# Kernel optimization log

Hardware: AMD Instinct MI355X
Metric: run time of the kernel (lower is better)

The kernel has to match this reference:

```python
import jax, jax.numpy as jnp
import numpy as np

S_SCALE = 40.0  # ReuseThreshold default s
EPS = 0.0  # torch .norm division has no eps; keep faithful


def _monotonic_threshold(param):
    # get_monotonic_threshold with use_sigmoid=True: squash raw param into (0, 1)
    return jax.nn.sigmoid(param)


def setup_inputs() -> dict:
    key = jax.random.key(0)
    k1, k2, k3, k4, k5 = jax.random.split(key, 5)
    B, N, D = 16, 2048, 768
    return {
        "query_input": jax.random.normal(k1, (B, N, D), dtype=jnp.float32),
        "query_value": jax.random.normal(k2, (B, N, D), dtype=jnp.float32),
        "cached_input": jax.random.normal(k3, (B, N, D), dtype=jnp.float32),
        "cached_value": jax.random.normal(k4, (B, N, D), dtype=jnp.float32),
        "sim_threshold": jax.random.normal(k5, (N,), dtype=jnp.float32),
    }


def reference(query_input, query_value, cached_input, cached_value, sim_threshold):
    # L2-normalize along feature dim
    nq = query_input / jnp.linalg.norm(query_input, axis=-1, keepdims=True)
    nc = cached_input / jnp.linalg.norm(cached_input, axis=-1, keepdims=True)
    # full similarity matrix [B, N, N], top-1 retrieval
    sim = jnp.einsum("bnd,bmd->bnm", nq, nc)
    most_similar_score = jnp.max(sim, axis=-1)          # [B, N]
    most_similar_idx = jnp.argmax(sim, axis=-1)         # [B, N]
    idx = most_similar_idx[..., None]                   # [B, N, 1]
    similar_input = jnp.take_along_axis(cached_input, idx, axis=1)  # [B, N, D]
    similar_value = jnp.take_along_axis(cached_value, idx, axis=1)
    # learned sigmoid threshold blend
    threshold = _monotonic_threshold(sim_threshold)     # [N]
    reuse_map = jax.nn.sigmoid(S_SCALE * (most_similar_score - threshold))  # [B, N]
    rm = reuse_map[..., None]
    reuse_input = (1.0 - rm) * query_input + rm * similar_input
    reuse_value = (1.0 - rm) * query_value + rm * similar_value
    return (reuse_map, reuse_input, reuse_value)
```

## Files before the change

kernel.cpp:

```cpp
#include <hip/hip_runtime.h>
#include <stdint.h>

#define BB 16
#define NN 2048
#define DD 768
#define BN (BB*NN)
#define NCH (DD/32)


typedef __attribute__((ext_vector_type(8))) short bf16x8;
typedef __attribute__((ext_vector_type(4))) float f32x4;

__device__ __forceinline__ ushort f2bf_rne(float x) {
    uint32_t u = __float_as_uint(x);
    u += 0x7fffu + ((u >> 16) & 1u);
    return (ushort)(u >> 16);
}

__device__ __forceinline__ void gload16(const void* g, void* l) {
    __builtin_amdgcn_global_load_lds(
        (const __attribute__((address_space(1))) void*)g,
        (__attribute__((address_space(3))) void*)l,
        16, 0, 0);
}

__global__ __launch_bounds__(256) void normconv_kernel(
        const float* __restrict__ qi, const float* __restrict__ ci,
        ushort* __restrict__ qh, ushort* __restrict__ ql,
        ushort* __restrict__ ch, ushort* __restrict__ cl) {
    const int gw   = blockIdx.x * 4 + (threadIdx.x >> 6);
    const int lane = threadIdx.x & 63;
#pragma unroll
    for (int it = 0; it < 8; it++) {
        int row = gw + it * 8192;
        bool isq = row < BN;
        const float* src = isq ? qi : ci;
        int r = row & (BN - 1);
        const float4* p = (const float4*)(src + (size_t)r * DD);
        float4 v[3];
        float s = 0.0f;
#pragma unroll
        for (int k = 0; k < 3; k++) {
            v[k] = p[lane + 64 * k];
            s += v[k].x*v[k].x + v[k].y*v[k].y + v[k].z*v[k].z + v[k].w*v[k].w;
        }
#pragma unroll
        for (int off = 32; off; off >>= 1) s += __shfl_xor(s, off);
        float inv = 1.0f / sqrtf(s);
        ushort* dh = (isq ? qh : ch) + (size_t)r * DD;
        ushort* dl = (isq ? ql : cl) + (size_t)r * DD;
#pragma unroll
        for (int k = 0; k < 3; k++) {
            int f = lane + 64 * k;
            float n[4] = {v[k].x * inv, v[k].y * inv, v[k].z * inv, v[k].w * inv};
            ushort hs[4], ls[4];
#pragma unroll
            for (int e = 0; e < 4; e++) {
                hs[e] = f2bf_rne(n[e]);
                ls[e] = f2bf_rne(n[e] - __uint_as_float((uint32_t)hs[e] << 16));
            }
            uint2 hv, lv;
            hv.x = (uint32_t)hs[0] | ((uint32_t)hs[1] << 16);
            hv.y = (uint32_t)hs[2] | ((uint32_t)hs[3] << 16);
            lv.x = (uint32_t)ls[0] | ((uint32_t)ls[1] << 16);
            lv.y = (uint32_t)ls[2] | ((uint32_t)ls[3] << 16);
            *(uint2*)(dh + 4 * (size_t)f) = hv;
            *(uint2*)(dl + 4 * (size_t)f) = lv;
        }
    }
}

__global__ __launch_bounds__(256, 2) void simmax_kernel(
        const ushort* __restrict__ qh, const ushort* __restrict__ ql,
        const ushort* __restrict__ ch, const ushort* __restrict__ cl,
        float* __restrict__ pmax, int* __restrict__ pidx) {
    __shared__ ushort smem[2][4][128 * 32];
    __shared__ float  redm[2][128];
    __shared__ int    redi[2][128];

    const int t  = threadIdx.x;
    const int l  = t & 63, wid = t >> 6;
    const int wy = wid >> 1, wx = wid & 1;
    const int fr = l & 15,  fs = l >> 4;
    const int n0 = blockIdx.x * 128;
    const int ms = blockIdx.y;
    const int b  = blockIdx.z;
    const int n0g = b * NN + n0;

    const int rowl = l >> 2;
    const int gs   = (l & 3) ^ ((l >> 3) & 3);
    const int rb   = wid * 32;

    const int swz = (fs ^ ((fr >> 1) & 3)) * 8;
    const int ra0 = (wy * 64 + fr) * 32 + swz;
    const int rb0 = (wx * 64 + fr) * 32 + swz;

    const ushort* srcs[4] = {qh, ql, ch, cl};

    float rmax[16]; int ridx[16];
#pragma unroll
    for (int k = 0; k < 16; k++) { rmax[k] = -3.0e38f; ridx[k] = 0; }

    for (int mt = ms; mt < 16; mt += 4) {
        const int m0  = mt * 128;
        const int m0g = b * NN + m0;

        f32x4 acc[4][4];
#pragma unroll
        for (int i = 0; i < 4; i++)
#pragma unroll
            for (int j = 0; j < 4; j++)
#pragma unroll
                for (int r = 0; r < 4; r++) acc[i][j][r] = 0.0f;

#pragma unroll
        for (int a = 0; a < 4; a++) {
            const ushort* sp = srcs[a]
                + (size_t)((a < 2 ? n0g : m0g) + rb + rowl) * DD + gs * 8;
            ushort* lp = &smem[0][a][rb * 32];
            gload16(sp, lp);
            gload16(sp + 16 * DD, lp + 16 * 32);
        }
        __syncthreads();

        int cur = 0;
        for (int c = 0; c < NCH; c++) {
            if (c + 1 < NCH) {
                const int k1 = (c + 1) * 32;
#pragma unroll
                for (int a = 0; a < 4; a++) {
                    const ushort* sp = srcs[a]
                        + (size_t)((a < 2 ? n0g : m0g) + rb + rowl) * DD
                        + k1 + gs * 8;
                    ushort* lp = &smem[cur ^ 1][a][rb * 32];
                    gload16(sp, lp);
                    gload16(sp + 16 * DD, lp + 16 * 32);
                }
            }
            bf16x8 ah[4], al[4], bhf[4], blf[4];
#pragma unroll
            for (int i = 0; i < 4; i++) {
                ah[i]  = *(const bf16x8*)&smem[cur][0][ra0 + i * 512];
                al[i]  = *(const bf16x8*)&smem[cur][1][ra0 + i * 512];
                bhf[i] = *(const bf16x8*)&smem[cur][2][rb0 + i * 512];
                blf[i] = *(const bf16x8*)&smem[cur][3][rb0 + i * 512];
            }
#pragma unroll
            for (int i = 0; i < 4; i++)
#pragma unroll
                for (int j = 0; j < 4; j++) {
                    asm("v_mfma_f32_16x16x32_bf16 %0, %1, %2, %0"
                        : "+v"(acc[i][j]) : "v"(ah[i]), "v"(bhf[j]));
                    asm("v_mfma_f32_16x16x32_bf16 %0, %1, %2, %0"
                        : "+v"(acc[i][j]) : "v"(al[i]), "v"(bhf[j]));
                    asm("v_mfma_f32_16x16x32_bf16 %0, %1, %2, %0"
                        : "+v"(acc[i][j]) : "v"(ah[i]), "v"(blf[j]));
                }
            __syncthreads();
            cur ^= 1;
        }

#pragma unroll
        for (int j = 0; j < 4; j++) {
            const int col = m0 + wx * 64 + j * 16 + fr;
#pragma unroll
            for (int i = 0; i < 4; i++)
#pragma unroll
                for (int r = 0; r < 4; r++) {
                    float val = acc[i][j][r];
                    int k = i * 4 + r;
                    if (val > rmax[k]) { rmax[k] = val; ridx[k] = col; }
                }
        }
    }

#pragma unroll
    for (int k = 0; k < 16; k++) {
        float m = rmax[k]; int id2 = ridx[k];
#pragma unroll
        for (int off = 1; off < 16; off <<= 1) {
            float om = __shfl_xor(m, off);
            int   oi = __shfl_xor(id2, off);
            if (om > m || (om == m && oi < id2)) { m = om; id2 = oi; }
        }
        if (fr == 0) {
            int r_loc = wy * 64 + (k >> 2) * 16 + fs * 4 + (k & 3);
            redm[wx][r_loc] = m;
            redi[wx][r_loc] = id2;
        }
    }
    __syncthreads();
    if (t < 128) {
        float m0v = redm[0][t]; int i0 = redi[0][t];
        float m1v = redm[1][t]; int i1 = redi[1][t];
        if (m1v > m0v || (m1v == m0v && i1 < i0)) { m0v = m1v; i0 = i1; }
        pmax[(b * 4 + ms) * NN + n0 + t] = m0v;
        pidx[(b * 4 + ms) * NN + n0 + t] = i0;
    }
}

__global__ __launch_bounds__(256) void blend_kernel(
        const float* __restrict__ qi, const float* __restrict__ qv,
        const float* __restrict__ ci, const float* __restrict__ cv,
        const float* __restrict__ pmax, const int* __restrict__ pidx,
        const float* __restrict__ st,
        float* __restrict__ out_map,
        float* __restrict__ out_ri, float* __restrict__ out_rv) {
    const int gw   = blockIdx.x * 4 + (threadIdx.x >> 6);
    const int lane = threadIdx.x & 63;

    float pm[4]; int pi[4];
    {
        int b = gw >> 11, n = gw & 2047;
#pragma unroll
        for (int s = 0; s < 4; s++) {
            pm[s] = pmax[(b * 4 + s) * NN + n];
            pi[s] = pidx[(b * 4 + s) * NN + n];
        }
    }

#pragma unroll
    for (int i = 0; i < 4; i++) {
        const int row = gw + i * 8192;
        const int b = row >> 11, n = row & 2047;

        float best = pm[0]; int bi = pi[0];
#pragma unroll
        for (int s = 1; s < 4; s++)
            if (pm[s] > best || (pm[s] == best && pi[s] < bi)) {
                best = pm[s]; bi = pi[s];
            }
        float thr = 1.0f / (1.0f + expf(-st[n]));
        float rm  = 1.0f / (1.0f + expf(-40.0f * (best - thr)));

        if (i < 3) {
            int rown = gw + (i + 1) * 8192;
            int bn_ = rown >> 11, nn_ = rown & 2047;
#pragma unroll
            for (int s = 0; s < 4; s++) {
                pm[s] = pmax[(bn_ * 4 + s) * NN + nn_];
                pi[s] = pidx[(bn_ * 4 + s) * NN + nn_];
            }
        }

        if (lane == 0) out_map[row] = rm;
        const float om = 1.0f - rm;
        const float4* q4 = (const float4*)(qi + (size_t)row * DD);
        const float4* v4 = (const float4*)(qv + (size_t)row * DD);
        const float4* s4 = (const float4*)(ci + ((size_t)b * NN + bi) * DD);
        const float4* w4 = (const float4*)(cv + ((size_t)b * NN + bi) * DD);
        float4* ori = (float4*)(out_ri + (size_t)row * DD);
        float4* orv = (float4*)(out_rv + (size_t)row * DD);
#pragma unroll
        for (int k = 0; k < 3; k++) {
            int f = lane + 64 * k;
            float4 a = q4[f], si = s4[f];
            float4 o;
            o.x = om * a.x + rm * si.x;
            o.y = om * a.y + rm * si.y;
            o.z = om * a.z + rm * si.z;
            o.w = om * a.w + rm * si.w;
            ori[f] = o;
            float4 av = v4[f], sv = w4[f];
            float4 p;
            p.x = om * av.x + rm * sv.x;
            p.y = om * av.y + rm * sv.y;
            p.z = om * av.z + rm * sv.z;
            p.w = om * av.w + rm * sv.w;
            orv[f] = p;
        }
    }
}

extern "C" void kernel_launch(void* const* d_in, const int* in_sizes, int n_in,
                              void* d_out, int out_size, void* d_ws, size_t ws_size,
                              hipStream_t stream) {
    const float* qi = (const float*)d_in[0];
    const float* qv = (const float*)d_in[1];
    const float* ci = (const float*)d_in[2];
    const float* cv = (const float*)d_in[3];
    const float* st = (const float*)d_in[4];

    float* ws    = (float*)d_ws;
    float* pmax  = ws;
    int*   pidx  = (int*)(ws + 131072);

    float* out     = (float*)d_out;
    float* out_map = out;
    float* out_ri  = out + 32768;
    float* out_rv  = out + 32768 + (size_t)BN * DD;

    ushort* qh = (ushort*)out_ri;
    ushort* ql = qh + (size_t)BN * DD;
    ushort* ch = (ushort*)out_rv;
    ushort* cl = ch + (size_t)BN * DD;

    normconv_kernel<<<2048, 256, 0, stream>>>(qi, ci, qh, ql, ch, cl);
    dim3 g2(16, 4, BB);
    simmax_kernel<<<g2, 256, 0, stream>>>(qh, ql, ch, cl, pmax, pidx);
    blend_kernel<<<2048, 256, 0, stream>>>(qi, qv, ci, cv, pmax, pidx, st,
                                           out_map, out_ri, out_rv);
}
```

Before: 821.2 us.

## Enlarge similarity GEMM tile to 256x256 with 8 waves and quarter-phased pipelining

The sim-max GEMM moves from 128x128 tiles with 4 waves to 256x256 tiles with 8 waves. Each K step is split into four MFMA phases, with the next tile's global-to-LDS loads interleaved between them, and s_setprio raised around the MFMA work. The prefetch now runs across M-tile boundaries so the pipeline does not drain between tiles. The larger tile halves global reloads per output and halves the number of M partials the blend kernel has to merge. In exchange it needs more registers and LDS per block, and the grid shrinks to 256 blocks, which may underfill the CUs.

```diff
diff --git a/kernel.cpp b/kernel.cpp
--- a/kernel.cpp
+++ b/kernel.cpp
@@ -5,7 +5,6 @@
 #define NN 2048
 #define DD 768
 #define BN (BB*NN)
-#define NCH (DD/32)
 
 
 typedef __attribute__((ext_vector_type(8))) short bf16x8;
@@ -70,133 +69,216 @@
     }
 }
 
-__global__ __launch_bounds__(256, 2) void simmax_kernel(
+__global__ __launch_bounds__(512, 2) void simmax_kernel(
         const ushort* __restrict__ qh, const ushort* __restrict__ ql,
         const ushort* __restrict__ ch, const ushort* __restrict__ cl,
         float* __restrict__ pmax, int* __restrict__ pidx) {
-    __shared__ ushort smem[2][4][128 * 32];
-    __shared__ float  redm[2][128];
-    __shared__ int    redi[2][128];
-
-    const int t  = threadIdx.x;
-    const int l  = t & 63, wid = t >> 6;
-    const int wy = wid >> 1, wx = wid & 1;
-    const int fr = l & 15,  fs = l >> 4;
-    const int n0 = blockIdx.x * 128;
-    const int ms = blockIdx.y;
-    const int b  = blockIdx.z;
+    __shared__ ushort sA[2][2][256 * 32];
+    __shared__ ushort sB[2][2][256 * 32];
+    __shared__ float  redm[4][256];
+    __shared__ int    redi[4][256];
+
+    const int t   = threadIdx.x;
+    const int l   = t & 63, wid = t >> 6;
+    const int wy  = wid >> 2, wx = wid & 3;
+    const int fr  = l & 15,  fs = l >> 4;
+    const int n0  = blockIdx.x * 256;
+    const int ms  = blockIdx.y;
+    const int b   = blockIdx.z;
     const int n0g = b * NN + n0;
 
     const int rowl = l >> 2;
     const int gs   = (l & 3) ^ ((l >> 3) & 3);
-    const int rb   = wid * 32;
-
-    const int swz = (fs ^ ((fr >> 1) & 3)) * 8;
-    const int ra0 = (wy * 64 + fr) * 32 + swz;
-    const int rb0 = (wx * 64 + fr) * 32 + swz;
-
-    const ushort* srcs[4] = {qh, ql, ch, cl};
-
-    float rmax[16]; int ridx[16];
-#pragma unroll
-    for (int k = 0; k < 16; k++) { rmax[k] = -3.0e38f; ridx[k] = 0; }
-
-    for (int mt = ms; mt < 16; mt += 4) {
-        const int m0  = mt * 128;
+    const int wr16 = wid * 16;
+
+    const int psl = (fs ^ ((fr >> 1) & 3)) * 8;
+    const int rA  = (wy * 128 + fr) * 32 + psl;
+    const int rB  = (wx * 64 + fr) * 32 + psl;
+
+    for (int u = t; u < 1024; u += 512) {
+        ((float*)redm)[u] = -3.0e38f;
+        ((int*)redi)[u]   = 0;
+    }
+
+#define STG(srcH, srcL, dH, dL, growbase, ko)                                \
+    {                                                                        \
+        const size_t off_ = (size_t)((growbase) + rowl) * DD + (ko) + gs * 8;\
+        gload16((srcH) + off_, (dH));                                        \
+        gload16((srcL) + off_, (dL));                                        \
+    }
+#define STG_A(nb, ih, ko) STG(qh, ql,                                        \
+        &sA[nb][0][((ih)*128 + wr16) * 32], &sA[nb][1][((ih)*128 + wr16)*32],\
+        n0g + (ih)*128 + wr16, ko)
+#define STG_B(nb, mh, m0gn, ko) STG(ch, cl,                                  \
+        &sB[nb][0][((mh)*128 + wr16) * 32], &sB[nb][1][((mh)*128 + wr16)*32],\
+        (m0gn) + (mh)*128 + wr16, ko)
+
+    {
+        const int m0gn = b * NN + ms * 256;
+        STG_A(0, 0, 0); STG_B(0, 0, m0gn, 0);
+        STG_A(0, 1, 0); STG_B(0, 1, m0gn, 0);
+    }
+    asm volatile("s_waitcnt vmcnt(0)" ::: "memory");
+    __builtin_amdgcn_s_barrier();
+    __builtin_amdgcn_sched_barrier(0);
+
+    int cur = 0;
+#pragma unroll 1
+    for (int q = 0; q < 4; q++) {
+        const int mt  = ms + 2 * q;
+        const int m0  = mt * 256;
         const int m0g = b * NN + m0;
 
-        f32x4 acc[4][4];
-#pragma unroll
-        for (int i = 0; i < 4; i++)
+        f32x4 acc[8][4];
+#pragma unroll
+        for (int i = 0; i < 8; i++)
 #pragma unroll
             for (int j = 0; j < 4; j++)
 #pragma unroll
                 for (int r = 0; r < 4; r++) acc[i][j][r] = 0.0f;
 
-#pragma unroll
-        for (int a = 0; a < 4; a++) {
-            const ushort* sp = srcs[a]
-                + (size_t)((a < 2 ? n0g : m0g) + rb + rowl) * DD + gs * 8;
-            ushort* lp = &smem[0][a][rb * 32];
-            gload16(sp, lp);
-            gload16(sp + 16 * DD, lp + 16 * 32);
-        }
-        __syncthreads();
-
-        int cur = 0;
-        for (int c = 0; c < NCH; c++) {
-            if (c + 1 < NCH) {
-                const int k1 = (c + 1) * 32;
-#pragma unroll
-                for (int a = 0; a < 4; a++) {
-                    const ushort* sp = srcs[a]
-                        + (size_t)((a < 2 ? n0g : m0g) + rb + rowl) * DD
-                        + k1 + gs * 8;
-                    ushort* lp = &smem[cur ^ 1][a][rb * 32];
-                    gload16(sp, lp);
-                    gload16(sp + 16 * DD, lp + 16 * 32);
-                }
-            }
-            bf16x8 ah[4], al[4], bhf[4], blf[4];
+        bf16x8 aH[4], aL[4];
+
+#pragma unroll 1
+        for (int kt = 0; kt < 24; kt++) {
+            const bool hasNext = !(q == 3 && kt == 23);
+            const int  kn      = (kt < 23) ? (kt + 1) * 32 : 0;
+            const int  m0gn    = (kt < 23) ? m0g : b * NN + (mt + 2) * 256;
+            const int  nb      = cur ^ 1;
+            bf16x8 bH[2], bL[2];
+
+            if (hasNext) { STG_A(nb, 0, kn); STG_B(nb, 0, m0gn, kn); }
 #pragma unroll
             for (int i = 0; i < 4; i++) {
-                ah[i]  = *(const bf16x8*)&smem[cur][0][ra0 + i * 512];
-                al[i]  = *(const bf16x8*)&smem[cur][1][ra0 + i * 512];
-                bhf[i] = *(const bf16x8*)&smem[cur][2][rb0 + i * 512];
-                blf[i] = *(const bf16x8*)&smem[cur][3][rb0 + i * 512];
-            }
+                aH[i] = *(const bf16x8*)&sA[cur][0][rA + i * 512];
+                aL[i] = *(const bf16x8*)&sA[cur][1][rA + i * 512];
+            }
+#pragma unroll
+            for (int j = 0; j < 2; j++) {
+                bH[j] = *(const bf16x8*)&sB[cur][0][rB + j * 512];
+                bL[j] = *(const bf16x8*)&sB[cur][1][rB + j * 512];
+            }
+            __builtin_amdgcn_s_setprio(1);
 #pragma unroll
             for (int i = 0; i < 4; i++)
 #pragma unroll
-                for (int j = 0; j < 4; j++) {
-                    asm("v_mfma_f32_16x16x32_bf16 %0, %1, %2, %0"
-                        : "+v"(acc[i][j]) : "v"(ah[i]), "v"(bhf[j]));
-                    asm("v_mfma_f32_16x16x32_bf16 %0, %1, %2, %0"
-                        : "+v"(acc[i][j]) : "v"(al[i]), "v"(bhf[j]));
-                    asm("v_mfma_f32_16x16x32_bf16 %0, %1, %2, %0"
-                        : "+v"(acc[i][j]) : "v"(ah[i]), "v"(blf[j]));
-                }
-            __syncthreads();
+                for (int j = 0; j < 2; j++) {
+                    asm("v_mfma_f32_16x16x32_bf16 %0, %1, %2, %0"
+                        : "+v"(acc[i][j]) : "v"(aH[i]), "v"(bH[j]));
+                    asm("v_mfma_f32_16x16x32_bf16 %0, %1, %2, %0"
+                        : "+v"(acc[i][j]) : "v"(aL[i]), "v"(bH[j]));
+                    asm("v_mfma_f32_16x16x32_bf16 %0, %1, %2, %0"
+                        : "+v"(acc[i][j]) : "v"(aH[i]), "v"(bL[j]));
+                }
+            __builtin_amdgcn_s_setprio(0);
+            __builtin_amdgcn_s_barrier();
+            __builtin_amdgcn_sched_barrier(0);
+
+            if (hasNext) { STG_A(nb, 1, kn); STG_B(nb, 1, m0gn, kn); }
+#pragma unroll
+            for (int j = 0; j < 2; j++) {
+                bH[j] = *(const bf16x8*)&sB[cur][0][rB + (2 + j) * 512];
+                bL[j] = *(const bf16x8*)&sB[cur][1][rB + (2 + j) * 512];
+            }
+            __builtin_amdgcn_s_setprio(1);
+#pragma unroll
+            for (int i = 0; i < 4; i++)
+#pragma unroll
+                for (int j = 0; j < 2; j++) {
+                    asm("v_mfma_f32_16x16x32_bf16 %0, %1, %2, %0"
+                        : "+v"(acc[i][2 + j]) : "v"(aH[i]), "v"(bH[j]));
+                    asm("v_mfma_f32_16x16x32_bf16 %0, %1, %2, %0"
+                        : "+v"(acc[i][2 + j]) : "v"(aL[i]), "v"(bH[j]));
+                    asm("v_mfma_f32_16x16x32_bf16 %0, %1, %2, %0"
+                        : "+v"(acc[i][2 + j]) : "v"(aH[i]), "v"(bL[j]));
+                }
+            __builtin_amdgcn_s_setprio(0);
+            __builtin_amdgcn_s_barrier();
+            __builtin_amdgcn_sched_barrier(0);
+
+#pragma unroll
+            for (int i = 0; i < 4; i++) {
+                aH[i] = *(const bf16x8*)&sA[cur][0][rA + 2048 + i * 512];
+                aL[i] = *(const bf16x8*)&sA[cur][1][rA + 2048 + i * 512];
+            }
+            __builtin_amdgcn_s_setprio(1);
+#pragma unroll
+            for (int i = 0; i < 4; i++)
+#pragma unroll
+                for (int j = 0; j < 2; j++) {
+                    asm("v_mfma_f32_16x16x32_bf16 %0, %1, %2, %0"
+                        : "+v"(acc[4 + i][2 + j]) : "v"(aH[i]), "v"(bH[j]));
+                    asm("v_mfma_f32_16x16x32_bf16 %0, %1, %2, %0"
+                        : "+v"(acc[4 + i][2 + j]) : "v"(aL[i]), "v"(bH[j]));
+                    asm("v_mfma_f32_16x16x32_bf16 %0, %1, %2, %0"
+                        : "+v"(acc[4 + i][2 + j]) : "v"(aH[i]), "v"(bL[j]));
+                }
+            __builtin_amdgcn_s_setprio(0);
+            __builtin_amdgcn_s_barrier();
+            __builtin_amdgcn_sched_barrier(0);
+
+#pragma unroll
+            for (int j = 0; j < 2; j++) {
+                bH[j] = *(const bf16x8*)&sB[cur][0][rB + j * 512];
+                bL[j] = *(const bf16x8*)&sB[cur][1][rB + j * 512];
+            }
+            __builtin_amdgcn_s_setprio(1);
+#pragma unroll
+            for (int i = 0; i < 4; i++)
+#pragma unroll
+                for (int j = 0; j < 2; j++) {
+                    asm("v_mfma_f32_16x16x32_bf16 %0, %1, %2, %0"
+                        : "+v"(acc[4 + i][j]) : "v"(aH[i]), "v"(bH[j]));
+                    asm("v_mfma_f32_16x16x32_bf16 %0, %1, %2, %0"
+                        : "+v"(acc[4 + i][j]) : "v"(aL[i]), "v"(bH[j]));
+                    asm("v_mfma_f32_16x16x32_bf16 %0, %1, %2, %0"
+                        : "+v"(acc[4 + i][j]) : "v"(aH[i]), "v"(bL[j]));
+                }
+            __builtin_amdgcn_s_setprio(0);
+            asm volatile("s_waitcnt vmcnt(0)" ::: "memory");
+            __builtin_amdgcn_s_barrier();
+            __builtin_amdgcn_sched_barrier(0);
             cur ^= 1;
         }
 
 #pragma unroll
-        for (int j = 0; j < 4; j++) {
-            const int col = m0 + wx * 64 + j * 16 + fr;
-#pragma unroll
-            for (int i = 0; i < 4; i++)
-#pragma unroll
-                for (int r = 0; r < 4; r++) {
-                    float val = acc[i][j][r];
-                    int k = i * 4 + r;
-                    if (val > rmax[k]) { rmax[k] = val; ridx[k] = col; }
-                }
-        }
-    }
-
-#pragma unroll
-    for (int k = 0; k < 16; k++) {
-        float m = rmax[k]; int id2 = ridx[k];
-#pragma unroll
-        for (int off = 1; off < 16; off <<= 1) {
-            float om = __shfl_xor(m, off);
-            int   oi = __shfl_xor(id2, off);
-            if (om > m || (om == m && oi < id2)) { m = om; id2 = oi; }
-        }
-        if (fr == 0) {
-            int r_loc = wy * 64 + (k >> 2) * 16 + fs * 4 + (k & 3);
-            redm[wx][r_loc] = m;
-            redi[wx][r_loc] = id2;
-        }
-    }
+        for (int i = 0; i < 8; i++)
+#pragma unroll
+            for (int r = 0; r < 4; r++) {
+                float m = acc[i][0][r];
+                int  id = m0 + wx * 64 + fr;
+#pragma unroll
+                for (int j = 1; j < 4; j++) {
+                    float v = acc[i][j][r];
+                    if (v > m) { m = v; id = m0 + wx * 64 + j * 16 + fr; }
+                }
+#pragma unroll
+                for (int off = 1; off < 16; off <<= 1) {
+                    float om = __shfl_xor(m, off);
+                    int   oi = __shfl_xor(id, off);
+                    if (om > m || (om == m && oi < id)) { m = om; id = oi; }
+                }
+                if (fr == 0) {
+                    int rw = wy * 128 + i * 16 + fs * 4 + r;
+                    if (m > redm[wx][rw]) { redm[wx][rw] = m; redi[wx][rw] = id; }
+                }
+            }
+    }
+
     __syncthreads();
-    if (t < 128) {
-        float m0v = redm[0][t]; int i0 = redi[0][t];
-        float m1v = redm[1][t]; int i1 = redi[1][t];
-        if (m1v > m0v || (m1v == m0v && i1 < i0)) { m0v = m1v; i0 = i1; }
-        pmax[(b * 4 + ms) * NN + n0 + t] = m0v;
-        pidx[(b * 4 + ms) * NN + n0 + t] = i0;
-    }
+    if (t < 256) {
+        float bm = redm[0][t]; int bi2 = redi[0][t];
+#pragma unroll
+        for (int s = 1; s < 4; s++) {
+            float p2 = redm[s][t]; int q2 = redi[s][t];
+            if (p2 > bm || (p2 == bm && q2 < bi2)) { bm = p2; bi2 = q2; }
+        }
+        pmax[(b * 2 + ms) * NN + n0 + t] = bm;
+        pidx[(b * 2 + ms) * NN + n0 + t] = bi2;
+    }
+#undef STG
+#undef STG_A
+#undef STG_B
 }
 
 __global__ __launch_bounds__(256) void blend_kernel(
@@ -209,13 +291,13 @@
     const int gw   = blockIdx.x * 4 + (threadIdx.x >> 6);
     const int lane = threadIdx.x & 63;
 
-    float pm[4]; int pi[4];
+    float pm[2]; int pi[2];
     {
         int b = gw >> 11, n = gw & 2047;
 #pragma unroll
-        for (int s = 0; s < 4; s++) {
-            pm[s] = pmax[(b * 4 + s) * NN + n];
-            pi[s] = pidx[(b * 4 + s) * NN + n];
+        for (int s = 0; s < 2; s++) {
+            pm[s] = pmax[(b * 2 + s) * NN + n];
+            pi[s] = pidx[(b * 2 + s) * NN + n];
         }
     }
 
@@ -225,11 +307,7 @@
         const int b = row >> 11, n = row & 2047;
 
         float best = pm[0]; int bi = pi[0];
-#pragma unroll
-        for (int s = 1; s < 4; s++)
-            if (pm[s] > best || (pm[s] == best && pi[s] < bi)) {
-                best = pm[s]; bi = pi[s];
-            }
+        if (pm[1] > best || (pm[1] == best && pi[1] < bi)) { best = pm[1]; bi = pi[1]; }
         float thr = 1.0f / (1.0f + expf(-st[n]));
         float rm  = 1.0f / (1.0f + expf(-40.0f * (best - thr)));
 
@@ -237,9 +315,9 @@
             int rown = gw + (i + 1) * 8192;
             int bn_ = rown >> 11, nn_ = rown & 2047;
 #pragma unroll
-            for (int s = 0; s < 4; s++) {
-                pm[s] = pmax[(bn_ * 4 + s) * NN + nn_];
-                pi[s] = pidx[(bn_ * 4 + s) * NN + nn_];
+            for (int s = 0; s < 2; s++) {
+                pm[s] = pmax[(bn_ * 2 + s) * NN + nn_];
+                pi[s] = pidx[(bn_ * 2 + s) * NN + nn_];
             }
         }
 
@@ -283,7 +361,7 @@
 
     float* ws    = (float*)d_ws;
     float* pmax  = ws;
-    int*   pidx  = (int*)(ws + 131072);
+    int*   pidx  = (int*)(ws + 65536);
 
     float* out     = (float*)d_out;
     float* out_map = out;
@@ -296,8 +374,8 @@
     ushort* cl = ch + (size_t)BN * DD;
 
     normconv_kernel<<<2048, 256, 0, stream>>>(qi, ci, qh, ql, ch, cl);
-    dim3 g2(16, 4, BB);
-    simmax_kernel<<<g2, 256, 0, stream>>>(qh, ql, ch, cl, pmax, pidx);
+    dim3 g2(8, 2, BB);
+    simmax_kernel<<<g2, 512, 0, stream>>>(qh, ql, ch, cl, pmax, pidx);
     blend_kernel<<<2048, 256, 0, stream>>>(qi, qv, ci, cv, pmax, pidx, st,
                                            out_map, out_ri, out_rv);
 }
```

New measurement: 891.5 us. 1.09x slower.
